# Kernel optimization log

Measured on AMD Instinct MI355X. Metric: run time of the kernel, lower is better.

## Reference

```python
import jax, jax.numpy as jnp
import numpy as np
from jax import lax

D_MODEL = 768; DEPTH = 12; HEADS = 12; HEAD_D = 64; PATCH = 16; IMG = 224
NTOK = (IMG // PATCH) ** 2 + 1  # 197
BATCH = 32; K_PATCHES = 5; EPS = 1e-6


def setup_inputs() -> dict:
    key = jax.random.key(0)
    ks = jax.random.split(key, 16)
    rn = lambda i, shape, s=1.0: jax.random.normal(ks[i], shape, jnp.float32) * s
    return {
        'x': rn(0, (BATCH, 3, IMG, IMG)),
        'patch_w': rn(1, (D_MODEL, 3, PATCH, PATCH), 0.02),
        'patch_b': jnp.zeros((D_MODEL,), jnp.float32),
        'cls_token': rn(2, (1, 1, D_MODEL), 0.02),
        'pos_embed': rn(3, (1, NTOK, D_MODEL), 0.02),
        'ln1_w': jnp.ones((DEPTH, D_MODEL), jnp.float32),
        'ln1_b': jnp.zeros((DEPTH, D_MODEL), jnp.float32),
        'qkv_w': rn(4, (DEPTH, 3 * D_MODEL, D_MODEL), 0.02),
        'qkv_b': jnp.zeros((DEPTH, 3 * D_MODEL), jnp.float32),
        'proj_w': rn(5, (DEPTH, D_MODEL, D_MODEL), 0.02),
        'proj_b': jnp.zeros((DEPTH, D_MODEL), jnp.float32),
        'pk_param': rn(6, (DEPTH, HEADS, HEAD_D), 0.02),
        'pv_param': rn(7, (DEPTH, HEADS, HEAD_D), 0.02),
        'prompt_k': rn(8, (DEPTH, HEADS, HEAD_D), 0.02),
        'prompt_v': rn(9, (DEPTH, HEADS, HEAD_D), 0.02),
        'ln2_w': jnp.ones((DEPTH, D_MODEL), jnp.float32),
        'ln2_b': jnp.zeros((DEPTH, D_MODEL), jnp.float32),
        'fc1_w': rn(10, (DEPTH, 4 * D_MODEL, D_MODEL), 0.02),
        'fc1_b': jnp.zeros((DEPTH, 4 * D_MODEL), jnp.float32),
        'fc2_w': rn(11, (DEPTH, D_MODEL, 4 * D_MODEL), 0.02),
        'fc2_b': jnp.zeros((DEPTH, D_MODEL), jnp.float32),
        'norm_w': jnp.ones((D_MODEL,), jnp.float32),
        'norm_b': jnp.zeros((D_MODEL,), jnp.float32),
        'k_patches': K_PATCHES,
    }


def _layer_norm(h, w, b):
    mu = h.mean(-1, keepdims=True)
    var = ((h - mu) ** 2).mean(-1, keepdims=True)
    return (h - mu) * lax.rsqrt(var + EPS) * w + b


def reference(x, patch_w, patch_b, cls_token, pos_embed, ln1_w, ln1_b, qkv_w, qkv_b,
              proj_w, proj_b, pk_param, pv_param, prompt_k, prompt_v, ln2_w, ln2_b,
              fc1_w, fc1_b, fc2_w, fc2_b, norm_w, norm_b, k_patches):
    B = x.shape[0]
    C, H, D = D_MODEL, HEADS, HEAD_D
    scale = D ** -0.5
    # patch embedding: conv stride=patch -> [B, C, 14, 14] -> [B, 196, C]
    p = lax.conv_general_dilated(x, patch_w, (PATCH, PATCH), 'VALID',
                                 dimension_numbers=('NCHW', 'OIHW', 'NCHW'))
    p = p.reshape(B, C, -1).transpose(0, 2, 1) + patch_b
    tokens = jnp.concatenate([jnp.broadcast_to(cls_token, (B, 1, C)), p], axis=1) + pos_embed
    N = tokens.shape[1]
    batch_idx = jnp.arange(B)[:, None]

    for l in range(DEPTH):
        h = _layer_norm(tokens, ln1_w[l], ln1_b[l])
        qkv = (h @ qkv_w[l].T + qkv_b[l]).reshape(B, N, 3, H, D).transpose(2, 0, 3, 1, 4)
        q, k, v = qkv[0], qkv[1], qkv[2]  # [B,H,N,D]
        # probe attention: softmax is row-wise, only the CLS row is used downstream
        probe = jax.nn.softmax(jnp.einsum('bhd,bhkd->bhk', q[:, :, 0], k) * scale, axis=-1)
        cls_scores = probe.mean(axis=1)[:, 1:]  # [B, N-1]
        topk_idx = lax.top_k(cls_scores, k_patches)[1] + 1  # [B, k] in [1, N)
        sel = jnp.zeros((B, N), tokens.dtype).at[batch_idx, topk_idx].add(1.0)  # [B,N]
        # prompt override of CLS k/v + scatter-add of learned patch prompts at top-k patches
        k_mod = k.at[:, :, 0, :].add(prompt_k[l]) + sel[:, None, :, None] * pk_param[l][None, :, None, :]
        v_mod = v.at[:, :, 0, :].add(prompt_v[l]) + sel[:, None, :, None] * pv_param[l][None, :, None, :]
        attn = jax.nn.softmax(jnp.einsum('bhqd,bhkd->bhqk', q, k_mod) * scale, axis=-1)
        out = jnp.einsum('bhqk,bhkd->bhqd', attn, v_mod).transpose(0, 2, 1, 3).reshape(B, N, C)
        tokens = tokens + (out @ proj_w[l].T + proj_b[l])
        h2 = _layer_norm(tokens, ln2_w[l], ln2_b[l])
        m = jax.nn.gelu(h2 @ fc1_w[l].T + fc1_b[l], approximate=False) @ fc2_w[l].T + fc2_b[l]
        tokens = tokens + m

    return _layer_norm(tokens, norm_w, norm_b)
```

## Files before the change

kernel.cpp:

```cpp
#include <hip/hip_runtime.h>
#include <math.h>

#define DMODEL 768
#define DEPTH 12
#define HEADS 12
#define HEADD 64
#define NTOK 197
#define BATCH 32
#define NPATCH 196
#define MTOK (BATCH * NTOK)
#define MPAT (BATCH * NPATCH)
#define QKVD 2304
#define MLPD 3072

typedef unsigned short u16;
typedef __attribute__((ext_vector_type(8))) short bf16x8;
typedef __attribute__((ext_vector_type(4))) float f32x4;

#define OFF_QKV 0
#define OFF_PROJ (QKVD * DMODEL)
#define OFF_FC1 (OFF_PROJ + DMODEL * DMODEL)
#define OFF_FC2 (OFF_FC1 + MLPD * DMODEL)
#define WTOTAL (OFF_FC2 + DMODEL * MLPD)

__device__ __forceinline__ u16 bf16r(float x) {
  union { float f; unsigned u; } c; c.f = x;
  unsigned u = c.u + 0x7FFF + ((c.u >> 16) & 1);
  return (u16)(u >> 16);
}
__device__ __forceinline__ float bf2f(u16 h) {
  union { unsigned u; float f; } c;
  c.u = (unsigned)h << 16;
  return c.f;
}
__device__ __forceinline__ float gelu_f(float x) {
  return 0.5f * x * (1.f + erff(x * 0.70710678118654752440f));
}
__device__ __forceinline__ void gload16(const void* g, void* l) {
  __builtin_amdgcn_global_load_lds(
      (const __attribute__((address_space(1))) void*)g,
      (__attribute__((address_space(3))) void*)l, 16, 0, 0);
}

__device__ __forceinline__ float blk_red_sum(float v, float* red) {
#pragma unroll
  for (int o = 32; o; o >>= 1) v += __shfl_xor(v, o);
  __syncthreads();
  if ((threadIdx.x & 63) == 0) red[threadIdx.x >> 6] = v;
  __syncthreads();
  return red[0] + red[1] + red[2] + red[3];
}
__device__ __forceinline__ float blk_red_max(float v, float* red) {
#pragma unroll
  for (int o = 32; o; o >>= 1) v = fmaxf(v, __shfl_xor(v, o));
  __syncthreads();
  if ((threadIdx.x & 63) == 0) red[threadIdx.x >> 6] = v;
  __syncthreads();
  return fmaxf(fmaxf(red[0], red[1]), fmaxf(red[2], red[3]));
}

__global__ __launch_bounds__(256) void convert_bf16(const float* __restrict__ in,
                                                    u16* __restrict__ out, int n) {
  int i = (blockIdx.x * 256 + threadIdx.x) * 4;
  if (i >= n) return;
  float4 v = *(const float4*)(in + i);
  ushort4 o;
  o.x = bf16r(v.x); o.y = bf16r(v.y); o.z = bf16r(v.z); o.w = bf16r(v.w);
  *(ushort4*)(out + i) = o;
}

__global__ __launch_bounds__(256) void convert_layer_w(
    const float* __restrict__ qkv_w, const float* __restrict__ proj_w,
    const float* __restrict__ fc1_w, const float* __restrict__ fc2_w,
    u16* __restrict__ wbuf) {
  int i = (blockIdx.x * 256 + threadIdx.x) * 4;
  if (i >= WTOTAL) return;
  const float* s;
  if (i < OFF_PROJ) s = qkv_w + i;
  else if (i < OFF_FC1) s = proj_w + (i - OFF_PROJ);
  else if (i < OFF_FC2) s = fc1_w + (i - OFF_FC1);
  else s = fc2_w + (i - OFF_FC2);
  float4 v = *(const float4*)s;
  ushort4 o;
  o.x = bf16r(v.x); o.y = bf16r(v.y); o.z = bf16r(v.z); o.w = bf16r(v.w);
  *(ushort4*)(wbuf + i) = o;
}

__global__ __launch_bounds__(256) void convert_all_w(
    const float* __restrict__ qkv_w, const float* __restrict__ proj_w,
    const float* __restrict__ fc1_w, const float* __restrict__ fc2_w,
    u16* __restrict__ wall) {
  const int l = blockIdx.y;
  int i = (blockIdx.x * 256 + threadIdx.x) * 4;
  if (i >= WTOTAL) return;
  const float* s;
  if (i < OFF_PROJ) s = qkv_w + (size_t)l * QKVD * DMODEL + i;
  else if (i < OFF_FC1) s = proj_w + (size_t)l * DMODEL * DMODEL + (i - OFF_PROJ);
  else if (i < OFF_FC2) s = fc1_w + (size_t)l * MLPD * DMODEL + (i - OFF_FC1);
  else s = fc2_w + (size_t)l * DMODEL * MLPD + (i - OFF_FC2);
  float4 v = *(const float4*)s;
  ushort4 o;
  o.x = bf16r(v.x); o.y = bf16r(v.y); o.z = bf16r(v.z); o.w = bf16r(v.w);
  *(ushort4*)(wall + (size_t)l * WTOTAL + i) = o;
}

__global__ __launch_bounds__(256) void im2col(const float* __restrict__ x,
                                              u16* __restrict__ col) {
  int idx = blockIdx.x * 256 + threadIdx.x;
  if (idx >= MPAT * DMODEL) return;
  int kk = idx % DMODEL;
  int m = idx / DMODEL;
  int bb = m / NPATCH, p = m % NPATCH;
  int ph = p / 14, pw = p % 14;
  int ch = kk >> 8, rem = kk & 255;
  int i = rem >> 4, j = rem & 15;
  col[idx] = bf16r(x[(((size_t)bb * 3 + ch) * 224 + ph * 16 + i) * 224 + pw * 16 + j]);
}

__global__ __launch_bounds__(256) void assemble(const float* __restrict__ pat,
                                                const float* __restrict__ cls,
                                                const float* __restrict__ pos,
                                                float* __restrict__ tokens) {
  int idx = blockIdx.x * 256 + threadIdx.x;
  if (idx >= MTOK * DMODEL) return;
  int c = idx % DMODEL;
  int t = idx / DMODEL;
  int bb = t / NTOK, n = t % NTOK;
  float v;
  if (n == 0) v = cls[c];
  else v = pat[((size_t)bb * NPATCH + (n - 1)) * DMODEL + c];
  tokens[idx] = v + pos[n * DMODEL + c];
}

template <bool BF16OUT>
__global__ __launch_bounds__(256) void layernorm_w(const float* __restrict__ in,
                                                   const float* __restrict__ w,
                                                   const float* __restrict__ b,
                                                   void* __restrict__ outp,
                                                   int ntok) {
  const int wv = threadIdx.x >> 6, lane = threadIdx.x & 63;
  const int t = blockIdx.x * 4 + wv;
  if (t >= ntok) return;
  const f32x4* r = (const f32x4*)(in + (size_t)t * DMODEL);
  f32x4 x0 = r[lane], x1 = r[lane + 64], x2 = r[lane + 128];
  float s = (x0[0] + x0[1] + x0[2] + x0[3]) + (x1[0] + x1[1] + x1[2] + x1[3]) +
            (x2[0] + x2[1] + x2[2] + x2[3]);
#pragma unroll
  for (int o = 32; o; o >>= 1) s += __shfl_xor(s, o);
  const float mu = s * (1.f / 768.f);
  float vs = 0.f;
#pragma unroll
  for (int e = 0; e < 4; ++e) {
    float d0 = x0[e] - mu, d1 = x1[e] - mu, d2 = x2[e] - mu;
    vs += d0 * d0 + d1 * d1 + d2 * d2;
  }
#pragma unroll
  for (int o = 32; o; o >>= 1) vs += __shfl_xor(vs, o);
  const float is = rsqrtf(vs * (1.f / 768.f) + 1e-6f);
  const f32x4* wp = (const f32x4*)w;
  const f32x4* bp = (const f32x4*)b;
  f32x4 w0 = wp[lane], w1 = wp[lane + 64], w2 = wp[lane + 128];
  f32x4 b0 = bp[lane], b1 = bp[lane + 64], b2 = bp[lane + 128];
  f32x4 y0, y1, y2;
#pragma unroll
  for (int e = 0; e < 4; ++e) {
    y0[e] = (x0[e] - mu) * is * w0[e] + b0[e];
    y1[e] = (x1[e] - mu) * is * w1[e] + b1[e];
    y2[e] = (x2[e] - mu) * is * w2[e] + b2[e];
  }
  if (BF16OUT) {
    ushort4* o = (ushort4*)((u16*)outp + (size_t)t * DMODEL);
    ushort4 q0, q1, q2;
#pragma unroll
    for (int e = 0; e < 4; ++e) {
      ((u16*)&q0)[e] = bf16r(y0[e]);
      ((u16*)&q1)[e] = bf16r(y1[e]);
      ((u16*)&q2)[e] = bf16r(y2[e]);
    }
    o[lane] = q0; o[lane + 64] = q1; o[lane + 128] = q2;
  } else {
    f32x4* o = (f32x4*)((float*)outp + (size_t)t * DMODEL);
    o[lane] = y0; o[lane + 64] = y1; o[lane + 128] = y2;
  }
}

template <int MODE, int TN>
__global__ __launch_bounds__(256) void gemm3(const u16* __restrict__ A,
                                             const u16* __restrict__ B,
                                             const float* __restrict__ bias,
                                             void* __restrict__ C,
                                             int M, int N, int K) {
  constexpr int NJ = TN / 32;
  constexpr int LPT = (TN == 128) ? 4 : 3;
  __shared__ u16 As[3][128 * 32];
  __shared__ u16 Bs[3][TN * 32];
  const int tid = threadIdx.x;
  const int w = tid >> 6, lane = tid & 63;

  const int nwg = gridDim.x * gridDim.y;
  int lin = blockIdx.y * gridDim.x + blockIdx.x;
  {
    int q = nwg >> 3, r = nwg & 7;
    int xcd = lin & 7, idx = lin >> 3;
    lin = (xcd < r ? xcd * (q + 1) : r * (q + 1) + (xcd - r) * q) + idx;
  }
  const int ntn = gridDim.y;
  const int m0 = (lin / ntn) * 128, n0 = (lin % ntn) * TN;

  const int wr = (w >> 1) * 64, wc = (w & 1) * (TN / 2);
  f32x4 acc[4][NJ] = {};

  const int srow = tid >> 2;
  const int scol = ((tid & 3) ^ ((srow >> 1) & 3)) * 8;
  int ar0 = m0 + srow;       if (ar0 >= M) ar0 = M - 1;
  int ar1 = m0 + 64 + srow;  if (ar1 >= M) ar1 = M - 1;
  const u16* Ag0 = A + (size_t)ar0 * K + scol;
  const u16* Ag1 = A + (size_t)ar1 * K + scol;
  const u16* Bg0 = B + (size_t)(n0 + srow) * K + scol;
  const u16* Bg1 = B + (size_t)(n0 + (TN == 128 ? 64 : 0) + srow) * K + scol;

  auto STAGE = [&](int buf, int kk) {
    gload16(Ag0 + kk, &As[buf][w * 512]);
    gload16(Ag1 + kk, &As[buf][2048 + w * 512]);
    gload16(Bg0 + kk, &Bs[buf][w * 512]);
    if (TN == 128) gload16(Bg1 + kk, &Bs[buf][2048 + w * 512]);
  };

  const int fr = lane & 15, lq = lane >> 4;
  const int kq = (lq ^ ((fr >> 1) & 3)) * 8;

  const int nt = K >> 5;
  STAGE(0, 0);
  STAGE(1, 32);
  asm volatile("s_waitcnt vmcnt(%0)" ::"n"(LPT) : "memory");
  __builtin_amdgcn_s_barrier();
  __builtin_amdgcn_sched_barrier(0);

  for (int t = 0; t < nt; ++t) {
    const int cur = t % 3;
    bf16x8 af[4], bfr[NJ];
#pragma unroll
    for (int i = 0; i < 4; ++i)
      af[i] = *(const bf16x8*)&As[cur][(wr + i * 16 + fr) * 32 + kq];
#pragma unroll
    for (int j = 0; j < NJ; ++j)
      bfr[j] = *(const bf16x8*)&Bs[cur][(wc + j * 16 + fr) * 32 + kq];
    const bool more = (t + 2 < nt);
    if (more) STAGE((t + 2) % 3, (t + 2) * 32);
#pragma unroll
    for (int i = 0; i < 4; ++i)
#pragma unroll
      for (int j = 0; j < NJ; ++j)
        acc[i][j] = __builtin_amdgcn_mfma_f32_16x16x32_bf16(af[i], bfr[j],
                                                            acc[i][j], 0, 0, 0);
    if (more)
      asm volatile("s_waitcnt vmcnt(%0)" ::"n"(LPT) : "memory");
    else
      asm volatile("s_waitcnt vmcnt(0)" ::: "memory");
    __builtin_amdgcn_s_barrier();
    __builtin_amdgcn_sched_barrier(0);
  }

  const int fq = lq * 4;
#pragma unroll
  for (int j = 0; j < NJ; ++j) {
    const int n = n0 + wc + j * 16 + fr;
    const float bb = bias[n];
#pragma unroll
    for (int i = 0; i < 4; ++i) {
      const int mbase = m0 + wr + i * 16 + fq;
#pragma unroll
      for (int r = 0; r < 4; ++r) {
        const int m = mbase + r;
        if (m < M) {
          const float v = acc[i][j][r] + bb;
          if (MODE == 0) ((float*)C)[(size_t)m * N + n] = v;
          else if (MODE == 1) ((float*)C)[(size_t)m * N + n] += v;
          else if (MODE == 2) ((u16*)C)[(size_t)m * N + n] = bf16r(gelu_f(v));
          else ((u16*)C)[(size_t)m * N + n] = bf16r(v);
        }
      }
    }
  }
}

__global__ __launch_bounds__(256) void probe_scores(const u16* __restrict__ qkv,
                                                    float* __restrict__ probs) {
  __shared__ float qrow[64];
  __shared__ float s[NTOK];
  __shared__ float red[4];
  const int bh = blockIdx.x;
  const int b = bh / HEADS, h = bh % HEADS;
  const int tid = threadIdx.x;
  const size_t row0 = (size_t)b * NTOK * QKVD;
  if (tid < 64) qrow[tid] = bf2f(qkv[row0 + h * HEADD + tid]);
  __syncthreads();
  const int sub = tid & 3;
  for (int k = tid >> 2; k < NTOK; k += 64) {
    const u16* kr = qkv + row0 + (size_t)k * QKVD + DMODEL + h * HEADD + sub * 16;
    bf16x8 k0 = *(const bf16x8*)kr;
    bf16x8 k1 = *(const bf16x8*)(kr + 8);
    float dot = 0.f;
#pragma unroll
    for (int e = 0; e < 8; ++e) {
      dot = fmaf(qrow[sub * 16 + e], bf2f((u16)k0[e]), dot);
      dot = fmaf(qrow[sub * 16 + 8 + e], bf2f((u16)k1[e]), dot);
    }
    dot += __shfl_xor(dot, 1);
    dot += __shfl_xor(dot, 2);
    if (sub == 0) s[k] = dot * 0.125f;
  }
  __syncthreads();
  float mx = -1e30f;
  for (int k = tid; k < NTOK; k += 256) mx = fmaxf(mx, s[k]);
  mx = blk_red_max(mx, red);
  float sm = 0.f;
  for (int k = tid; k < NTOK; k += 256) sm += expf(s[k] - mx);
  sm = blk_red_sum(sm, red);
  float inv = 1.f / sm;
  for (int k = tid; k < NTOK; k += 256)
    probs[(size_t)bh * NTOK + k] = expf(s[k] - mx) * inv;
}

__global__ __launch_bounds__(256) void topk_sel(const float* __restrict__ probs,
                                                const int* __restrict__ kpptr,
                                                int* __restrict__ topk) {
  __shared__ float accsc[NTOK];
  const int b = blockIdx.x, tid = threadIdx.x;
  for (int k = tid; k < NTOK; k += 256) {
    float a = 0.f;
#pragma unroll
    for (int h = 0; h < HEADS; ++h) a += probs[(size_t)(b * HEADS + h) * NTOK + k];
    accsc[k] = a;
  }
  __syncthreads();
  if (tid == 0) {
    int kpn = kpptr[0];
    if (kpn < 0) kpn = 0;
    if (kpn > 8) kpn = 8;
    for (int j = 0; j < kpn; ++j) {
      float best = -1e30f;
      int bi = 1;
      for (int k = 1; k < NTOK; ++k)
        if (accsc[k] > best) { best = accsc[k]; bi = k; }
      topk[b * 8 + j] = bi;
      accsc[bi] = -2e30f;
    }
    for (int j = kpn; j < 8; ++j) topk[b * 8 + j] = -1;
  }
}

__global__ __launch_bounds__(512, 1) void attn_mfma(
    const u16* __restrict__ qkv, const float* __restrict__ prompt_k,
    const float* __restrict__ prompt_v, const float* __restrict__ pk,
    const float* __restrict__ pv, const int* __restrict__ topk,
    const int* __restrict__ kpptr, u16* __restrict__ outp) {
  __shared__ u16 Ks[208 * 64];
  __shared__ u16 Vs[64 * 256];
  __shared__ u16 Ps[8][16 * 256];
  __shared__ float selb[NTOK];
  const int bh = blockIdx.x;
  const int b = bh / HEADS, h = bh % HEADS;
  const int tid = threadIdx.x, w = tid >> 6, lane = tid & 63;
  const int fr = lane & 15, lq = lane >> 4;

  int kpn = kpptr[0];
  if (kpn < 0) kpn = 0;
  if (kpn > 8) kpn = 8;
  for (int k = tid; k < NTOK; k += 512) {
    float sl = 0.f;
    for (int j = 0; j < kpn; ++j)
      if (topk[b * 8 + j] == k) sl = 1.f;
    selb[k] = sl;
  }
  __syncthreads();

  const size_t row0 = (size_t)b * NTOK * QKVD;
  const u16* kg = qkv + row0 + DMODEL + h * HEADD;
  const u16* vg = qkv + row0 + 2 * DMODEL + h * HEADD;
  for (int idx = tid; idx < 208 * 64; idx += 512) {
    int tok = idx >> 6, d = idx & 63;
    float v = 0.f;
    if (tok < NTOK) {
      v = bf2f(kg[(size_t)tok * QKVD + d]) + selb[tok] * pk[h * HEADD + d];
      if (tok == 0) v += prompt_k[h * HEADD + d];
    }
    int off = (tok * 128 + d * 2) ^ ((tok & 7) << 4);
    *(u16*)((char*)Ks + off) = bf16r(v);
  }
  for (int idx = tid; idx < 224 * 64; idx += 512) {
    int tok = idx >> 6, d = idx & 63;
    float v = 0.f;
    if (tok < NTOK) {
      v = bf2f(vg[(size_t)tok * QKVD + d]) + selb[tok] * pv[h * HEADD + d];
      if (tok == 0) v += prompt_v[h * HEADD + d];
    }
    int off = (d * 512 + tok * 2) ^ ((d & 7) << 4);
    *(u16*)((char*)Vs + off) = bf16r(v);
  }
  __syncthreads();

  u16* Pw = Ps[w];
  u16* ob = outp + (size_t)b * NTOK * DMODEL + h * HEADD;

#pragma unroll
  for (int pass = 0; pass < 2; ++pass) {
    const int qt = pass * 8 + w;
    const bool active = (qt < 14);
    if (active) {
      int qrow = qt * 16 + fr;
      if (qrow > NTOK - 1) qrow = NTOK - 1;
      const u16* qp = qkv + row0 + (size_t)qrow * QKVD + h * HEADD + lq * 8;
      bf16x8 aq0 = *(const bf16x8*)qp;
      bf16x8 aq1 = *(const bf16x8*)(qp + 32);
      f32x4 sa[13];
#pragma unroll
      for (int j = 0; j < 13; ++j) {
        int tok = j * 16 + fr;
        int o0 = (tok * 128 + lq * 16) ^ ((tok & 7) << 4);
        int o1 = (tok * 128 + 64 + lq * 16) ^ ((tok & 7) << 4);
        bf16x8 bk0 = *(const bf16x8*)((const char*)Ks + o0);
        bf16x8 bk1 = *(const bf16x8*)((const char*)Ks + o1);
        f32x4 z = {0.f, 0.f, 0.f, 0.f};
        z = __builtin_amdgcn_mfma_f32_16x16x32_bf16(aq0, bk0, z, 0, 0, 0);
        sa[j] = __builtin_amdgcn_mfma_f32_16x16x32_bf16(aq1, bk1, z, 0, 0, 0);
      }
      const bool v12 = (fr < 5);
      float m4[4] = {-1e30f, -1e30f, -1e30f, -1e30f};
#pragma unroll
      for (int j = 0; j < 13; ++j) {
        if (j == 12 && !v12) continue;
#pragma unroll
        for (int r = 0; r < 4; ++r) m4[r] = fmaxf(m4[r], sa[j][r] * 0.125f);
      }
#pragma unroll
      for (int o = 8; o; o >>= 1)
#pragma unroll
        for (int r = 0; r < 4; ++r) m4[r] = fmaxf(m4[r], __shfl_xor(m4[r], o));
      float s4[4] = {0.f, 0.f, 0.f, 0.f};
#pragma unroll
      for (int j = 0; j < 13; ++j) {
        const bool valid = (j < 12) || v12;
#pragma unroll
        for (int r = 0; r < 4; ++r) {
          float p = valid ? __expf(sa[j][r] * 0.125f - m4[r]) : 0.f;
          sa[j][r] = p;
          s4[r] += p;
        }
      }
#pragma unroll
      for (int o = 8; o; o >>= 1)
#pragma unroll
        for (int r = 0; r < 4; ++r) s4[r] += __shfl_xor(s4[r], o);
      float inv[4];
#pragma unroll
      for (int r = 0; r < 4; ++r) inv[r] = 1.f / s4[r];
#pragma unroll
      for (int r = 0; r < 4; ++r) {
        int row = lq * 4 + r;
        int rbase = row * 512, sw = (row & 7) << 4;
#pragma unroll
        for (int j = 0; j < 13; ++j) {
          int off = (rbase + (j * 16 + fr) * 2) ^ sw;
          *(u16*)((char*)Pw + off) = bf16r(sa[j][r] * inv[r]);
        }
        int offz = (rbase + (208 + fr) * 2) ^ sw;
        *(u16*)((char*)Pw + offz) = 0;
      }
    }
    __syncthreads();
    if (active) {
      f32x4 oa[4] = {};
#pragma unroll
      for (int kc = 0; kc < 7; ++kc) {
        int po = (fr * 512 + (kc * 32 + lq * 8) * 2) ^ ((fr & 7) << 4);
        bf16x8 pa = *(const bf16x8*)((const char*)Pw + po);
#pragma unroll
        for (int dt = 0; dt < 4; ++dt) {
          int d = dt * 16 + fr;
          int vo = (d * 512 + (kc * 32 + lq * 8) * 2) ^ ((d & 7) << 4);
          bf16x8 vb = *(const bf16x8*)((const char*)Vs + vo);
          oa[dt] = __builtin_amdgcn_mfma_f32_16x16x32_bf16(pa, vb, oa[dt], 0, 0, 0);
        }
      }
#pragma unroll
      for (int r = 0; r < 4; ++r) {
        int q = qt * 16 + lq * 4 + r;
        if (q < NTOK) {
          u16* orow = ob + (size_t)q * DMODEL;
#pragma unroll
          for (int dt = 0; dt < 4; ++dt) orow[dt * 16 + fr] = bf16r(oa[dt][r]);
        }
      }
    }
    __syncthreads();
  }
}

extern "C" void kernel_launch(void* const* d_in, const int* in_sizes, int n_in,
                              void* d_out, int out_size, void* d_ws, size_t ws_size,
                              hipStream_t stream) {
  const float* x = (const float*)d_in[0];
  const float* patch_w = (const float*)d_in[1];
  const float* patch_b = (const float*)d_in[2];
  const float* cls_tok = (const float*)d_in[3];
  const float* pos_emb = (const float*)d_in[4];
  const float* ln1_w = (const float*)d_in[5];
  const float* ln1_b = (const float*)d_in[6];
  const float* qkv_w = (const float*)d_in[7];
  const float* qkv_b = (const float*)d_in[8];
  const float* proj_w = (const float*)d_in[9];
  const float* proj_b = (const float*)d_in[10];
  const float* pk_par = (const float*)d_in[11];
  const float* pv_par = (const float*)d_in[12];
  const float* pr_k = (const float*)d_in[13];
  const float* pr_v = (const float*)d_in[14];
  const float* ln2_w = (const float*)d_in[15];
  const float* ln2_b = (const float*)d_in[16];
  const float* fc1_w = (const float*)d_in[17];
  const float* fc1_b = (const float*)d_in[18];
  const float* fc2_w = (const float*)d_in[19];
  const float* fc2_b = (const float*)d_in[20];
  const float* norm_w = (const float*)d_in[21];
  const float* norm_b = (const float*)d_in[22];
  const int* kp = (const int*)d_in[23];

  char* base = (char*)d_ws;
  float* tokens = (float*)base;
  float* bufh = (float*)(base + 19365888ull);
  float* bufbig = (float*)(base + 38731776ull);
  u16* im2colb = (u16*)(base + 116195328ull);
  u16* patchwb = (u16*)(base + 125829120ull);
  int* topk = (int*)(base + 127008768ull);
  float* probs = (float*)(base + 127009792ull);
  u16* wbuf = (u16*)(base + 127312384ull);
  const size_t WBYTES = (size_t)WTOTAL * 2;
  const bool batch = ws_size >= 127312384ull + WBYTES * DEPTH;

  const int mt = (MTOK + 127) / 128;
  const int mtp = (MPAT + 127) / 128;
  const int lnb = (MTOK + 3) / 4;

  if (batch)
    convert_all_w<<<dim3(WTOTAL / 1024, DEPTH), 256, 0, stream>>>(
        qkv_w, proj_w, fc1_w, fc2_w, wbuf);

  convert_bf16<<<(DMODEL * DMODEL / 4 + 255) / 256, 256, 0, stream>>>(
      patch_w, patchwb, DMODEL * DMODEL);
  im2col<<<(MPAT * DMODEL + 255) / 256, 256, 0, stream>>>(x, im2colb);
  gemm3<0, 64><<<dim3(mtp, DMODEL / 64), 256, 0, stream>>>(
      im2colb, patchwb, patch_b, bufh, MPAT, DMODEL, DMODEL);
  assemble<<<(MTOK * DMODEL + 255) / 256, 256, 0, stream>>>(bufh, cls_tok,
                                                            pos_emb, tokens);

  for (int l = 0; l < DEPTH; ++l) {
    u16* wl = batch ? (wbuf + (size_t)l * WTOTAL) : wbuf;
    if (!batch)
      convert_layer_w<<<(WTOTAL / 4 + 255) / 256, 256, 0, stream>>>(
          qkv_w + (size_t)l * QKVD * DMODEL,
          proj_w + (size_t)l * DMODEL * DMODEL,
          fc1_w + (size_t)l * MLPD * DMODEL,
          fc2_w + (size_t)l * DMODEL * MLPD, wl);
    layernorm_w<true><<<lnb, 256, 0, stream>>>(tokens, ln1_w + l * DMODEL,
                                               ln1_b + l * DMODEL, bufh, MTOK);
    gemm3<3, 128><<<dim3(mt, QKVD / 128), 256, 0, stream>>>(
        (const u16*)bufh, wl + OFF_QKV, qkv_b + l * QKVD, bufbig,
        MTOK, QKVD, DMODEL);
    probe_scores<<<BATCH * HEADS, 256, 0, stream>>>((const u16*)bufbig, probs);
    topk_sel<<<BATCH, 256, 0, stream>>>(probs, kp, topk);
    attn_mfma<<<BATCH * HEADS, 512, 0, stream>>>(
        (const u16*)bufbig, pr_k + l * HEADS * HEADD, pr_v + l * HEADS * HEADD,
        pk_par + l * HEADS * HEADD, pv_par + l * HEADS * HEADD, topk, kp,
        (u16*)bufh);
    gemm3<1, 64><<<dim3(mt, DMODEL / 64), 256, 0, stream>>>(
        (const u16*)bufh, wl + OFF_PROJ, proj_b + l * DMODEL, tokens,
        MTOK, DMODEL, DMODEL);
    layernorm_w<true><<<lnb, 256, 0, stream>>>(tokens, ln2_w + l * DMODEL,
                                               ln2_b + l * DMODEL, bufh, MTOK);
    gemm3<2, 128><<<dim3(mt, MLPD / 128), 256, 0, stream>>>(
        (const u16*)bufh, wl + OFF_FC1, fc1_b + l * MLPD, bufbig,
        MTOK, MLPD, DMODEL);
    gemm3<1, 64><<<dim3(mt, DMODEL / 64), 256, 0, stream>>>(
        (const u16*)bufbig, wl + OFF_FC2, fc2_b + l * DMODEL, tokens,
        MTOK, DMODEL, MLPD);
  }
  layernorm_w<false><<<lnb, 256, 0, stream>>>(tokens, norm_w, norm_b, d_out,
                                              MTOK);
}
```

Before: 3.740 ms.

## Use 8-wave GEMM tiles, fuse probe softmax with top-k, widen weight conversion

The GEMM moves from 4 waves per 256-thread block to 8 waves per 512-thread block on the same 128xTN tile. Each wave now owns a smaller sub-tile with fewer accumulators, and each thread issues one or two global-to-LDS loads per stage instead of three or four. This is meant to add waves that hide latency, at the cost of less register reuse per wave and more barrier participants. The probe-score and top-k kernels are merged into one block per batch with one wave per head, which drops the intermediate probs buffer and a launch. The weight conversion kernel now handles 8 elements per thread.

Result: faster. 3.500 ms (-6.4%).

```diff
diff --git a/kernel.cpp b/kernel.cpp
--- a/kernel.cpp
+++ b/kernel.cpp
@@ -49,14 +49,6 @@
   if ((threadIdx.x & 63) == 0) red[threadIdx.x >> 6] = v;
   __syncthreads();
   return red[0] + red[1] + red[2] + red[3];
-}
-__device__ __forceinline__ float blk_red_max(float v, float* red) {
-#pragma unroll
-  for (int o = 32; o; o >>= 1) v = fmaxf(v, __shfl_xor(v, o));
-  __syncthreads();
-  if ((threadIdx.x & 63) == 0) red[threadIdx.x >> 6] = v;
-  __syncthreads();
-  return fmaxf(fmaxf(red[0], red[1]), fmaxf(red[2], red[3]));
 }
 
 __global__ __launch_bounds__(256) void convert_bf16(const float* __restrict__ in,
@@ -91,17 +83,21 @@
     const float* __restrict__ fc1_w, const float* __restrict__ fc2_w,
     u16* __restrict__ wall) {
   const int l = blockIdx.y;
-  int i = (blockIdx.x * 256 + threadIdx.x) * 4;
+  int i = (blockIdx.x * 256 + threadIdx.x) * 8;
   if (i >= WTOTAL) return;
   const float* s;
   if (i < OFF_PROJ) s = qkv_w + (size_t)l * QKVD * DMODEL + i;
   else if (i < OFF_FC1) s = proj_w + (size_t)l * DMODEL * DMODEL + (i - OFF_PROJ);
   else if (i < OFF_FC2) s = fc1_w + (size_t)l * MLPD * DMODEL + (i - OFF_FC1);
   else s = fc2_w + (size_t)l * DMODEL * MLPD + (i - OFF_FC2);
-  float4 v = *(const float4*)s;
-  ushort4 o;
-  o.x = bf16r(v.x); o.y = bf16r(v.y); o.z = bf16r(v.z); o.w = bf16r(v.w);
-  *(ushort4*)(wall + (size_t)l * WTOTAL + i) = o;
+  float4 v0 = *(const float4*)s;
+  float4 v1 = *(const float4*)(s + 4);
+  ushort4 o0, o1;
+  o0.x = bf16r(v0.x); o0.y = bf16r(v0.y); o0.z = bf16r(v0.z); o0.w = bf16r(v0.w);
+  o1.x = bf16r(v1.x); o1.y = bf16r(v1.y); o1.z = bf16r(v1.z); o1.w = bf16r(v1.w);
+  u16* d = wall + (size_t)l * WTOTAL + i;
+  *(ushort4*)d = o0;
+  *(ushort4*)(d + 4) = o1;
 }
 
 __global__ __launch_bounds__(256) void im2col(const float* __restrict__ x,
@@ -185,13 +181,12 @@
 }
 
 template <int MODE, int TN>
-__global__ __launch_bounds__(256) void gemm3(const u16* __restrict__ A,
-                                             const u16* __restrict__ B,
-                                             const float* __restrict__ bias,
-                                             void* __restrict__ C,
-                                             int M, int N, int K) {
-  constexpr int NJ = TN / 32;
-  constexpr int LPT = (TN == 128) ? 4 : 3;
+__global__ __launch_bounds__(512, 4) void gemm8(const u16* __restrict__ A,
+                                                const u16* __restrict__ B,
+                                                const float* __restrict__ bias,
+                                                void* __restrict__ C,
+                                                int M, int N, int K) {
+  constexpr int NI = (TN == 128) ? 4 : 2;
   __shared__ u16 As[3][128 * 32];
   __shared__ u16 Bs[3][TN * 32];
   const int tid = threadIdx.x;
@@ -207,23 +202,21 @@
   const int ntn = gridDim.y;
   const int m0 = (lin / ntn) * 128, n0 = (lin % ntn) * TN;
 
-  const int wr = (w >> 1) * 64, wc = (w & 1) * (TN / 2);
-  f32x4 acc[4][NJ] = {};
+  const int wr = (TN == 128) ? (w >> 2) * 64 : (w >> 1) * 32;
+  const int wc = (TN == 128) ? (w & 3) * 32 : (w & 1) * 32;
+  f32x4 acc[NI][2] = {};
 
   const int srow = tid >> 2;
   const int scol = ((tid & 3) ^ ((srow >> 1) & 3)) * 8;
-  int ar0 = m0 + srow;       if (ar0 >= M) ar0 = M - 1;
-  int ar1 = m0 + 64 + srow;  if (ar1 >= M) ar1 = M - 1;
-  const u16* Ag0 = A + (size_t)ar0 * K + scol;
-  const u16* Ag1 = A + (size_t)ar1 * K + scol;
-  const u16* Bg0 = B + (size_t)(n0 + srow) * K + scol;
-  const u16* Bg1 = B + (size_t)(n0 + (TN == 128 ? 64 : 0) + srow) * K + scol;
+  int ar = m0 + srow;
+  if (ar >= M) ar = M - 1;
+  const u16* Ag = A + (size_t)ar * K + scol;
+  const u16* Bg = B + (size_t)(n0 + srow) * K + scol;
+  const bool doB = (TN == 128) || (w < 4);
 
   auto STAGE = [&](int buf, int kk) {
-    gload16(Ag0 + kk, &As[buf][w * 512]);
-    gload16(Ag1 + kk, &As[buf][2048 + w * 512]);
-    gload16(Bg0 + kk, &Bs[buf][w * 512]);
-    if (TN == 128) gload16(Bg1 + kk, &Bs[buf][2048 + w * 512]);
+    gload16(Ag + kk, &As[buf][w * 512]);
+    if (doB) gload16(Bg + kk, &Bs[buf][w * 512]);
   };
 
   const int fr = lane & 15, lq = lane >> 4;
@@ -232,42 +225,49 @@
   const int nt = K >> 5;
   STAGE(0, 0);
   STAGE(1, 32);
-  asm volatile("s_waitcnt vmcnt(%0)" ::"n"(LPT) : "memory");
+  if (doB)
+    asm volatile("s_waitcnt vmcnt(2)" ::: "memory");
+  else
+    asm volatile("s_waitcnt vmcnt(1)" ::: "memory");
   __builtin_amdgcn_s_barrier();
   __builtin_amdgcn_sched_barrier(0);
 
   for (int t = 0; t < nt; ++t) {
     const int cur = t % 3;
-    bf16x8 af[4], bfr[NJ];
-#pragma unroll
-    for (int i = 0; i < 4; ++i)
+    bf16x8 af[NI], bfr[2];
+#pragma unroll
+    for (int i = 0; i < NI; ++i)
       af[i] = *(const bf16x8*)&As[cur][(wr + i * 16 + fr) * 32 + kq];
 #pragma unroll
-    for (int j = 0; j < NJ; ++j)
+    for (int j = 0; j < 2; ++j)
       bfr[j] = *(const bf16x8*)&Bs[cur][(wc + j * 16 + fr) * 32 + kq];
     const bool more = (t + 2 < nt);
     if (more) STAGE((t + 2) % 3, (t + 2) * 32);
 #pragma unroll
-    for (int i = 0; i < 4; ++i)
-#pragma unroll
-      for (int j = 0; j < NJ; ++j)
+    for (int i = 0; i < NI; ++i)
+#pragma unroll
+      for (int j = 0; j < 2; ++j)
         acc[i][j] = __builtin_amdgcn_mfma_f32_16x16x32_bf16(af[i], bfr[j],
                                                             acc[i][j], 0, 0, 0);
-    if (more)
-      asm volatile("s_waitcnt vmcnt(%0)" ::"n"(LPT) : "memory");
-    else
+    if (more) {
+      if (doB)
+        asm volatile("s_waitcnt vmcnt(2)" ::: "memory");
+      else
+        asm volatile("s_waitcnt vmcnt(1)" ::: "memory");
+    } else {
       asm volatile("s_waitcnt vmcnt(0)" ::: "memory");
+    }
     __builtin_amdgcn_s_barrier();
     __builtin_amdgcn_sched_barrier(0);
   }
 
   const int fq = lq * 4;
 #pragma unroll
-  for (int j = 0; j < NJ; ++j) {
+  for (int j = 0; j < 2; ++j) {
     const int n = n0 + wc + j * 16 + fr;
     const float bb = bias[n];
 #pragma unroll
-    for (int i = 0; i < 4; ++i) {
+    for (int i = 0; i < NI; ++i) {
       const int mbase = m0 + wr + i * 16 + fq;
 #pragma unroll
       for (int r = 0; r < 4; ++r) {
@@ -284,54 +284,64 @@
   }
 }
 
-__global__ __launch_bounds__(256) void probe_scores(const u16* __restrict__ qkv,
-                                                    float* __restrict__ probs) {
-  __shared__ float qrow[64];
-  __shared__ float s[NTOK];
-  __shared__ float red[4];
-  const int bh = blockIdx.x;
-  const int b = bh / HEADS, h = bh % HEADS;
-  const int tid = threadIdx.x;
+__global__ __launch_bounds__(768) void probe_topk12(const u16* __restrict__ qkv,
+                                                    const int* __restrict__ kpptr,
+                                                    int* __restrict__ topk) {
+  __shared__ float qsh[HEADS][64];
+  __shared__ float pbuf[HEADS][NTOK];
+  __shared__ float accsc[NTOK];
+  const int b = blockIdx.x, tid = threadIdx.x;
+  const int h = tid >> 6, lane = tid & 63;
   const size_t row0 = (size_t)b * NTOK * QKVD;
-  if (tid < 64) qrow[tid] = bf2f(qkv[row0 + h * HEADD + tid]);
-  __syncthreads();
-  const int sub = tid & 3;
-  for (int k = tid >> 2; k < NTOK; k += 64) {
-    const u16* kr = qkv + row0 + (size_t)k * QKVD + DMODEL + h * HEADD + sub * 16;
-    bf16x8 k0 = *(const bf16x8*)kr;
-    bf16x8 k1 = *(const bf16x8*)(kr + 8);
+  qsh[h][lane] = bf2f(qkv[row0 + h * HEADD + lane]);
+  __syncthreads();
+  const int sub = lane & 3;
+  const int kbase = lane >> 2;
+  float p[13];
+  float smax = -1e30f;
+#pragma unroll
+  for (int i = 0; i < 13; ++i) {
+    const int k = kbase + i * 16;
     float dot = 0.f;
-#pragma unroll
-    for (int e = 0; e < 8; ++e) {
-      dot = fmaf(qrow[sub * 16 + e], bf2f((u16)k0[e]), dot);
-      dot = fmaf(qrow[sub * 16 + 8 + e], bf2f((u16)k1[e]), dot);
+    if (k < NTOK) {
+      const u16* kr = qkv + row0 + (size_t)k * QKVD + DMODEL + h * HEADD + sub * 16;
+      bf16x8 k0 = *(const bf16x8*)kr;
+      bf16x8 k1 = *(const bf16x8*)(kr + 8);
+#pragma unroll
+      for (int e = 0; e < 8; ++e) {
+        dot = fmaf(qsh[h][sub * 16 + e], bf2f((u16)k0[e]), dot);
+        dot = fmaf(qsh[h][sub * 16 + 8 + e], bf2f((u16)k1[e]), dot);
+      }
     }
     dot += __shfl_xor(dot, 1);
     dot += __shfl_xor(dot, 2);
-    if (sub == 0) s[k] = dot * 0.125f;
-  }
-  __syncthreads();
-  float mx = -1e30f;
-  for (int k = tid; k < NTOK; k += 256) mx = fmaxf(mx, s[k]);
-  mx = blk_red_max(mx, red);
-  float sm = 0.f;
-  for (int k = tid; k < NTOK; k += 256) sm += expf(s[k] - mx);
-  sm = blk_red_sum(sm, red);
-  float inv = 1.f / sm;
-  for (int k = tid; k < NTOK; k += 256)
-    probs[(size_t)bh * NTOK + k] = expf(s[k] - mx) * inv;
-}
-
-__global__ __launch_bounds__(256) void topk_sel(const float* __restrict__ probs,
-                                                const int* __restrict__ kpptr,
-                                                int* __restrict__ topk) {
-  __shared__ float accsc[NTOK];
-  const int b = blockIdx.x, tid = threadIdx.x;
-  for (int k = tid; k < NTOK; k += 256) {
+    p[i] = (k < NTOK) ? dot * 0.125f : -1e30f;
+    smax = fmaxf(smax, p[i]);
+  }
+#pragma unroll
+  for (int o = 32; o; o >>= 1) smax = fmaxf(smax, __shfl_xor(smax, o));
+  float ssum = 0.f;
+#pragma unroll
+  for (int i = 0; i < 13; ++i) {
+    p[i] = (p[i] > -1e29f) ? __expf(p[i] - smax) : 0.f;
+    ssum += p[i];
+  }
+#pragma unroll
+  for (int o = 32; o; o >>= 1) ssum += __shfl_xor(ssum, o);
+  const float inv = 4.f / ssum;
+  if (sub == 0) {
+#pragma unroll
+    for (int i = 0; i < 13; ++i) {
+      const int k = kbase + i * 16;
+      if (k < NTOK) pbuf[h][k] = p[i] * inv;
+    }
+  }
+  __syncthreads();
+  if (tid < NTOK) {
     float a = 0.f;
 #pragma unroll
-    for (int h = 0; h < HEADS; ++h) a += probs[(size_t)(b * HEADS + h) * NTOK + k];
-    accsc[k] = a;
+    for (int hh = 0; hh < HEADS; ++hh) a += pbuf[hh][tid];
+    accsc[tid] = a;
   }
   __syncthreads();
   if (tid == 0) {
@@ -532,7 +542,6 @@
   u16* im2colb = (u16*)(base + 116195328ull);
   u16* patchwb = (u16*)(base + 125829120ull);
   int* topk = (int*)(base + 127008768ull);
-  float* probs = (float*)(base + 127009792ull);
   u16* wbuf = (u16*)(base + 127312384ull);
   const size_t WBYTES = (size_t)WTOTAL * 2;
   const bool batch = ws_size >= 127312384ull + WBYTES * DEPTH;
@@ -542,13 +551,13 @@
   const int lnb = (MTOK + 3) / 4;
 
   if (batch)
-    convert_all_w<<<dim3(WTOTAL / 1024, DEPTH), 256, 0, stream>>>(
+    convert_all_w<<<dim3(WTOTAL / 2048, DEPTH), 256, 0, stream>>>(
         qkv_w, proj_w, fc1_w, fc2_w, wbuf);
 
   convert_bf16<<<(DMODEL * DMODEL / 4 + 255) / 256, 256, 0, stream>>>(
       patch_w, patchwb, DMODEL * DMODEL);
   im2col<<<(MPAT * DMODEL + 255) / 256, 256, 0, stream>>>(x, im2colb);
-  gemm3<0, 64><<<dim3(mtp, DMODEL / 64), 256, 0, stream>>>(
+  gemm8<0, 64><<<dim3(mtp, DMODEL / 64), 512, 0, stream>>>(
       im2colb, patchwb, patch_b, bufh, MPAT, DMODEL, DMODEL);
   assemble<<<(MTOK * DMODEL + 255) / 256, 256, 0, stream>>>(bufh, cls_tok,
                                                             pos_emb, tokens);
@@ -563,24 +572,23 @@
           fc2_w + (size_t)l * DMODEL * MLPD, wl);
     layernorm_w<true><<<lnb, 256, 0, stream>>>(tokens, ln1_w + l * DMODEL,
                                                ln1_b + l * DMODEL, bufh, MTOK);
-    gemm3<3, 128><<<dim3(mt, QKVD / 128), 256, 0, stream>>>(
+    gemm8<3, 128><<<dim3(mt, QKVD / 128), 512, 0, stream>>>(
         (const u16*)bufh, wl + OFF_QKV, qkv_b + l * QKVD, bufbig,
         MTOK, QKVD, DMODEL);
-    probe_scores<<<BATCH * HEADS, 256, 0, stream>>>((const u16*)bufbig, probs);
-    topk_sel<<<BATCH, 256, 0, stream>>>(probs, kp, topk);
+    probe_topk12<<<BATCH, 768, 0, stream>>>((const u16*)bufbig, kp, topk);
     attn_mfma<<<BATCH * HEADS, 512, 0, stream>>>(
         (const u16*)bufbig, pr_k + l * HEADS * HEADD, pr_v + l * HEADS * HEADD,
         pk_par + l * HEADS * HEADD, pv_par + l * HEADS * HEADD, topk, kp,
         (u16*)bufh);
-    gemm3<1, 64><<<dim3(mt, DMODEL / 64), 256, 0, stream>>>(
+    gemm8<1, 64><<<dim3(mt, DMODEL / 64), 512, 0, stream>>>(
         (const u16*)bufh, wl + OFF_PROJ, proj_b + l * DMODEL, tokens,
         MTOK, DMODEL, DMODEL);
     layernorm_w<true><<<lnb, 256, 0, stream>>>(tokens, ln2_w + l * DMODEL,
                                                ln2_b + l * DMODEL, bufh, MTOK);
-    gemm3<2, 128><<<dim3(mt, MLPD / 128), 256, 0, stream>>>(
+    gemm8<2, 128><<<dim3(mt, MLPD / 128), 512, 0, stream>>>(
         (const u16*)bufh, wl + OFF_FC1, fc1_b + l * MLPD, bufbig,
         MTOK, MLPD, DMODEL);
-    gemm3<1, 64><<<dim3(mt, DMODEL / 64), 256, 0, stream>>>(
+    gemm8<1, 64><<<dim3(mt, DMODEL / 64), 512, 0, stream>>>(
         (const u16*)bufbig, wl + OFF_FC2, fc2_b + l * DMODEL, tokens,
         MTOK, DMODEL, MLPD);
   }
```
